# Kernel tuning notes

Measured on AMD Instinct MI355X. Metric: run time of the kernel, lower is better.

The kernel has to match this reference:

```python
import jax, jax.numpy as jnp
import numpy as np

NMS_THR = 0.3


def pairwise_iou(b):
    # b: [N,4] in x1,y1,x2,y2
    area = (b[:, 2] - b[:, 0]) * (b[:, 3] - b[:, 1])  # [N]
    x1 = jnp.maximum(b[:, None, 0], b[None, :, 0])
    y1 = jnp.maximum(b[:, None, 1], b[None, :, 1])
    x2 = jnp.minimum(b[:, None, 2], b[None, :, 2])
    y2 = jnp.minimum(b[:, None, 3], b[None, :, 3])
    inter = jnp.clip(x2 - x1, 0.0) * jnp.clip(y2 - y1, 0.0)
    return inter / (area[:, None] + area[None, :] - inter + 1e-9)


def nms_keep(boxes, scores, valid, thr):
    # greedy NMS, fixed-shape: returns bool keep mask in original order
    N = boxes.shape[0]
    order = jnp.argsort(-jnp.where(valid, scores, -jnp.inf))
    b = boxes[order]
    v = valid[order]
    iou = pairwise_iou(b)  # [N,N]

    def step(keep, i):
        suppressed = jnp.any(keep & (iou[i] > thr))
        keep = keep.at[i].set(v[i] & jnp.logical_not(suppressed))
        return keep, None

    keep_sorted, _ = jax.lax.scan(step, jnp.zeros((N,), dtype=bool), jnp.arange(N))
    return jnp.zeros((N,), dtype=bool).at[order].set(keep_sorted)


def setup_inputs() -> dict:
    key = jax.random.key(0)
    k1, k2, k3, k4 = jax.random.split(key, 4)
    N, C, S = 6000, 81, 800
    # well-formed proposals: x1,y1 in [0, 600), w,h in [8, 200)
    xy = jax.random.uniform(k1, (N, 2), dtype=jnp.float32) * 600.0
    wh = 8.0 + jax.random.uniform(k2, (N, 2), dtype=jnp.float32) * 192.0
    proposals = jnp.concatenate([xy, xy + wh], axis=1)  # [N,4]
    reg = jax.random.normal(k3, (N, C * 4), dtype=jnp.float32)
    clss = jax.random.normal(k4, (N, C), dtype=jnp.float32) * 2.0
    stds = jnp.array([0.1, 0.1, 0.2, 0.2], dtype=jnp.float32)
    return {"proposals": proposals, "reg": reg, "clss": clss, "stds": stds, "img_size": S}


def reference(proposals, reg, clss, stds, img_size):
    N, C = clss.shape
    # anchors_bbox2offset: x1y1x2y2 -> center x,y + w,h
    w = proposals[:, 2] - proposals[:, 0]
    h = proposals[:, 3] - proposals[:, 1]
    cx = proposals[:, 0] + 0.5 * w
    cy = proposals[:, 1] + 0.5 * h
    # class selection
    probs = jax.nn.softmax(clss, axis=1)
    cls_idx = jnp.argmax(probs, axis=1)  # [N]
    score = jnp.take_along_axis(probs, cls_idx[:, None], axis=1)[:, 0]
    valid = cls_idx != 0  # non-background
    reg4 = reg.reshape(N, C, 4)
    t = jnp.take_along_axis(reg4, cls_idx[:, None, None], axis=1)[:, 0, :] * stds  # [N,4]
    # decode
    px = cx + w * t[:, 0]
    py = cy + h * t[:, 1]
    pw = w * jnp.exp(t[:, 2])
    ph = h * jnp.exp(t[:, 3])
    # offset2bbox + clip
    hi = jnp.float32(img_size - 1)
    x1 = jnp.clip(px - 0.5 * pw, 0.0, hi)
    y1 = jnp.clip(py - 0.5 * ph, 0.0, hi)
    x2 = jnp.clip(px + 0.5 * pw, 0.0, hi)
    y2 = jnp.clip(py + 0.5 * ph, 0.0, hi)
    boxes = jnp.stack((x1, y1, x2, y2), axis=1)  # [N,4]
    keep = nms_keep(jax.lax.stop_gradient(boxes), jax.lax.stop_gradient(score), valid, NMS_THR)
    m = keep.astype(boxes.dtype)
    return boxes * m[:, None], score * m, cls_idx * keep.astype(cls_idx.dtype)
```

## Files before the change

kernel.cpp:

```cpp
#include <hip/hip_runtime.h>
#include <math.h>

#define NMS_THR 0.3f
#define NACC 8

__device__ __forceinline__ float fmul(float a, float b){ return __fmul_rn(a,b); }
__device__ __forceinline__ float fadd(float a, float b){ return __fadd_rn(a,b); }
__device__ __forceinline__ float fsub(float a, float b){ return __fsub_rn(a,b); }

#define BAR_LDS() asm volatile("s_waitcnt lgkmcnt(0)\n\ts_barrier" ::: "memory")

__device__ __forceinline__ unsigned long long rfl64(unsigned long long x){
    unsigned int lo = (unsigned int)__builtin_amdgcn_readfirstlane((int)(unsigned int)x);
    unsigned int hi = (unsigned int)__builtin_amdgcn_readfirstlane((int)(unsigned int)(x >> 32));
    return ((unsigned long long)hi << 32) | lo;
}
__device__ __forceinline__ unsigned long long waveOr64(unsigned long long v){
    for (int o = 32; o > 0; o >>= 1) v |= __shfl_xor(v, o);
    return v;
}

__global__ __launch_bounds__(256) void k_decode(
    const float* __restrict__ prop, const float* __restrict__ reg,
    const float* __restrict__ clss, const float* __restrict__ stds,
    const int* __restrict__ imgsz,
    float* __restrict__ boxes, float* __restrict__ key,
    float* __restrict__ score, int* __restrict__ cls,
    int N, int C)
{
    int wid  = threadIdx.x >> 6;
    int lane = threadIdx.x & 63;
    int n = blockIdx.x * 4 + wid;
    if (n >= N) return;
    const float* row = clss + (long)n * C;
    float ninf = -__builtin_inff();
    float x0 = (lane < C)      ? row[lane]      : ninf;
    float x1 = (lane + 64 < C) ? row[lane + 64] : ninf;
    float m = fmaxf(x0, x1);
    for (int o = 32; o > 0; o >>= 1) m = fmaxf(m, __shfl_xor(m, o));
    float e0 = (lane < C)      ? expf(x0 - m) : 0.0f;
    float e1 = (lane + 64 < C) ? expf(x1 - m) : 0.0f;
    float s = e0 + e1;
    for (int o = 32; o > 0; o >>= 1) s += __shfl_xor(s, o);
    float bv; int bi;
    if (e0 >= e1) { bv = e0; bi = lane; } else { bv = e1; bi = lane + 64; }
    for (int o = 32; o > 0; o >>= 1) {
        float ov = __shfl_xor(bv, o);
        int   oi = __shfl_xor(bi, o);
        if (ov > bv || (ov == bv && oi < bi)) { bv = ov; bi = oi; }
    }
    if (lane == 0) {
        float sc = 1.0f / s;
        int   c  = bi;
        int   valid = (c != 0);
        float p0 = prop[n*4+0], p1 = prop[n*4+1], p2 = prop[n*4+2], p3 = prop[n*4+3];
        float w  = fsub(p2, p0), h = fsub(p3, p1);
        float cx = fadd(p0, fmul(0.5f, w));
        float cy = fadd(p1, fmul(0.5f, h));
        const float* rr = reg + (long)n * C * 4 + (long)c * 4;
        float t0 = fmul(rr[0], stds[0]);
        float t1 = fmul(rr[1], stds[1]);
        float t2 = fmul(rr[2], stds[2]);
        float t3 = fmul(rr[3], stds[3]);
        float px = fadd(cx, fmul(w, t0));
        float py = fadd(cy, fmul(h, t1));
        float pw = fmul(w, expf(t2));
        float ph = fmul(h, expf(t3));
        float hi = (float)(imgsz[0] - 1);
        float bx1 = fminf(fmaxf(fsub(px, fmul(0.5f, pw)), 0.0f), hi);
        float by1 = fminf(fmaxf(fsub(py, fmul(0.5f, ph)), 0.0f), hi);
        float bx2 = fminf(fmaxf(fadd(px, fmul(0.5f, pw)), 0.0f), hi);
        float by2 = fminf(fmaxf(fadd(py, fmul(0.5f, ph)), 0.0f), hi);
        boxes[n*4+0]=bx1; boxes[n*4+1]=by1; boxes[n*4+2]=bx2; boxes[n*4+3]=by2;
        score[n] = sc;
        cls[n]   = c;
        key[n]   = valid ? sc : ninf;
    }
}

__global__ __launch_bounds__(256) void k_rank(
    const float* __restrict__ key, const float* __restrict__ boxes,
    float* __restrict__ boxesSorted, float* __restrict__ areaSorted,
    float* __restrict__ keySorted, int* __restrict__ rank,
    int* __restrict__ nValidPtr, int N)
{
    extern __shared__ float lkey[];
    __shared__ int part[256];
    int tid = threadIdx.x;
    for (int j = tid; j < N; j += 256) lkey[j] = key[j];
    __syncthreads();

    int i = blockIdx.x * 64 + (tid & 63);
    int s = tid >> 6;
    int Q = (N + 3) >> 2;
    int r_part = 0;
    if (i < N) {
        float ki = lkey[i];
        int j0 = s * Q, j1 = min(N, j0 + Q);
        for (int j = j0; j < j1; ++j) {
            float kj = lkey[j];
            r_part += (kj > ki) || (kj == ki && j < i);
        }
    }
    part[tid] = r_part;
    __syncthreads();

    if (tid < 64 && i < N) {
        int r = part[tid] + part[tid+64] + part[tid+128] + part[tid+192];
        float ki = lkey[i];
        rank[i] = r;
        float b0 = boxes[i*4+0], b1 = boxes[i*4+1], b2 = boxes[i*4+2], b3 = boxes[i*4+3];
        boxesSorted[r*4+0]=b0; boxesSorted[r*4+1]=b1; boxesSorted[r*4+2]=b2; boxesSorted[r*4+3]=b3;
        areaSorted[r] = fmul(fsub(b2,b0), fsub(b3,b1));
        keySorted[r]  = ki;
    }

    if (blockIdx.x == 0) {
        __syncthreads();
        float ninf = -__builtin_inff();
        int inv = 0;
        for (int j = tid; j < N; j += 256) inv += (lkey[j] == ninf);
        part[tid] = inv;
        __syncthreads();
        if (tid == 0) {
            int t = 0;
            for (int q = 0; q < 256; ++q) t += part[q];
            nValidPtr[0] = N - t;
        }
    }
}

__global__ __launch_bounds__(256) void k_mask(
    const float* __restrict__ bs, const float* __restrict__ areas,
    const float* __restrict__ keySorted, unsigned long long* __restrict__ mask,
    unsigned long long* __restrict__ dq,
    unsigned long long* __restrict__ bdiag, unsigned long long* __restrict__ bprev,
    int N, int W, int Wpad)
{
    int wid  = threadIdx.x >> 6;
    int lane = threadIdx.x & 63;
    int i = blockIdx.x * 4 + wid;
    if (i >= N) return;
    if (keySorted[i] == -__builtin_inff()) return;
    float ax1 = bs[i*4+0], ay1 = bs[i*4+1], ax2 = bs[i*4+2], ay2 = bs[i*4+3];
    float aa  = areas[i];
    int w0 = i >> 6;
    if (lane == 0) {
        dq[i*4+0] = 0ULL; dq[i*4+1] = 0ULL; dq[i*4+2] = 0ULL; dq[i*4+3] = 0ULL;
    }
    if (w0 & 1) {
        int j = (w0 - 1) * 64 + lane;
        int bit = 0;
        if (j < N) {
            float bx1 = bs[j*4+0], by1 = bs[j*4+1], bx2 = bs[j*4+2], by2 = bs[j*4+3];
            float ba  = areas[j];
            float ix1 = fmaxf(ax1,bx1), iy1 = fmaxf(ay1,by1);
            float ix2 = fminf(ax2,bx2), iy2 = fminf(ay2,by2);
            float iw = fmaxf(fsub(ix2,ix1), 0.0f);
            float ih = fmaxf(fsub(iy2,iy1), 0.0f);
            float inter = fmul(iw, ih);
            float denom = fadd(fsub(fadd(aa, ba), inter), 1e-9f);
            float iou = inter / denom;
            bit = (iou > NMS_THR) ? 1 : 0;
        }
        unsigned long long bm = __ballot(bit);
        if (lane == 0) bprev[i] = bm;
    }
    for (int w = w0; w < W; ++w) {
        int j = w*64 + lane;
        int bit = 0;
        if (j < N && j != i) {
            float bx1 = bs[j*4+0], by1 = bs[j*4+1], bx2 = bs[j*4+2], by2 = bs[j*4+3];
            float ba  = areas[j];
            float ix1 = fmaxf(ax1,bx1), iy1 = fmaxf(ay1,by1);
            float ix2 = fminf(ax2,bx2), iy2 = fminf(ay2,by2);
            float iw = fmaxf(fsub(ix2,ix1), 0.0f);
            float ih = fmaxf(fsub(iy2,iy1), 0.0f);
            float inter = fmul(iw, ih);
            float denom = fadd(fsub(fadd(aa, ba), inter), 1e-9f);
            float iou = inter / denom;
            bit = (iou > NMS_THR) ? 1 : 0;
        }
        unsigned long long fwd = __ballot(bit && (j > i));
        if (w == w0) {
            unsigned long long bwd = __ballot(bit && (j < i));
            if (lane == 0) {
                mask[(long)i*Wpad + w] = fwd;
                dq[i*4+0] = fwd;
                bdiag[i]  = bwd;
            }
        } else {
            if (lane == 0) {
                mask[(long)i*Wpad + w] = fwd;
                int d = w - w0;
                if (d < 4) dq[i*4+d] = fwd;
            }
        }
    }
}

__global__ __launch_bounds__((NACC+1)*64, 1) void k_scan(
    const unsigned long long* __restrict__ mask,
    const unsigned long long* __restrict__ dq,
    const unsigned long long* __restrict__ bdiag,
    const unsigned long long* __restrict__ bprev,
    const int* __restrict__ nValidPtr,
    int* __restrict__ keepSorted, int N, int W, int Wpad)
{
    __shared__ unsigned long long ldsPartA[NACC+1];
    __shared__ unsigned long long ldsPartB[NACC+1];
    __shared__ unsigned long long ldsKeepLo, ldsKeepHi;
    int tid  = threadIdx.x;
    int wid  = tid >> 6;
    int lane = tid & 63;
    for (int i = tid; i < N; i += (NACC+1)*64) keepSorted[i] = 0;
    if (tid <= NACC) { ldsPartA[tid] = 0ULL; ldsPartB[tid] = 0ULL; }
    if (tid == 0) { ldsKeepLo = 0ULL; ldsKeepHi = 0ULL; }
    __syncthreads();

    int nValid  = __builtin_amdgcn_readfirstlane(nValidPtr[0]);
    int nChunks = (nValid + 127) >> 7;

    unsigned long long vA=0, vBp=0, vBd=0, A2=0, A3=0, B1=0, B2=0;
    unsigned long long sacc_prevA = 0ULL, sacc_prevB = 0ULL;
    if (wid == 0 && nChunks > 0) {
        int rA = lane, rB = 64 + lane;
        if (rA < N) {
            vA = bdiag[rA];
            ulonglong2 a23 = *(const ulonglong2*)(dq + (size_t)rA*4 + 2);
            A2 = a23.x; A3 = a23.y;
        }
        if (rB < N) {
            vBp = bprev[rB];
            vBd = bdiag[rB];
            ulonglong2 b01 = *(const ulonglong2*)(dq + (size_t)rB*4);
            ulonglong2 b23 = *(const ulonglong2*)(dq + (size_t)rB*4 + 2);
            B1 = b01.y; B2 = b23.x;
        }
    }
    unsigned long long accx = 0ULL, accy = 0ULL;
    bool accWave = (wid >= 1);
    int  accIdx  = wid - 1;
    bool laneok  = (2*lane + 1 < Wpad);

    for (int c = 0; c < nChunks; ++c) {
        int base = c << 7;
        if (wid == 0) {
            unsigned long long nvA=0, nvBp=0, nvBd=0, nA2=0, nA3=0, nB1=0, nB2=0;
            if (c + 1 < nChunks) {
                int rA = base + 128 + lane, rB = base + 192 + lane;
                if (rA < N) {
                    nvA = bdiag[rA];
                    ulonglong2 a23 = *(const ulonglong2*)(dq + (size_t)rA*4 + 2);
                    nA2 = a23.x; nA3 = a23.y;
                }
                if (rB < N) {
                    nvBp = bprev[rB];
                    nvBd = bdiag[rB];
                    ulonglong2 b01 = *(const ulonglong2*)(dq + (size_t)rB*4);
                    ulonglong2 b23 = *(const ulonglong2*)(dq + (size_t)rB*4 + 2);
                    nB1 = b01.y; nB2 = b23.x;
                }
            }

            unsigned long long pA = sacc_prevA, pB = sacc_prevB;
#pragma unroll
            for (int k = 1; k <= NACC; ++k) { pA |= ldsPartA[k]; pB |= ldsPartB[k]; }
            unsigned long long incLo = rfl64(pA), incHi = rfl64(pB);
            int nv  = nValid - base;
            unsigned long long validLo = (nv >= 64) ? ~0ULL : ((1ULL << nv) - 1ULL);
            int nv2 = nv - 64;
            unsigned long long validHi = (nv2 >= 64) ? ~0ULL
                                        : (nv2 <= 0 ? 0ULL : ((1ULL << nv2) - 1ULL));
            unsigned long long candLo = validLo & ~incLo;
            unsigned long long candHi = validHi & ~incHi;
            unsigned long long keepLo = 0ULL, keepHi = 0ULL;

            while (candLo) {
                int f = __builtin_ctzll(candLo);
                unsigned long long sup = __ballot(((vA >> f) & 1ULL) != 0ULL);
                unsigned long long b = 1ULL << f;
                keepLo |= b;
                candLo &= ~sup & ~b;
            }
            candHi &= ~__ballot((vBp & keepLo) != 0ULL);
            while (candHi) {
                int f = __builtin_ctzll(candHi);
                unsigned long long sup = __ballot(((vBd >> f) & 1ULL) != 0ULL);
                unsigned long long b = 1ULL << f;
                keepHi |= b;
                candHi &= ~sup & ~b;
            }
            {
                unsigned long long kL = (keepLo >> lane) & 1ULL;
                unsigned long long kH = (keepHi >> lane) & 1ULL;
                unsigned long long selA = (kL ? A2 : 0ULL) | (kH ? B1 : 0ULL);
                unsigned long long selB = (kL ? A3 : 0ULL) | (kH ? B2 : 0ULL);
                sacc_prevA = waveOr64(selA);
                sacc_prevB = waveOr64(selB);
            }
            if (lane == 0) { ldsKeepLo = keepLo; ldsKeepHi = keepHi; }
            if (base + lane < N)      keepSorted[base + lane]      = (int)((keepLo >> lane) & 1ULL);
            if (base + 64 + lane < N) keepSorted[base + 64 + lane] = (int)((keepHi >> lane) & 1ULL);
            vA=nvA; vBp=nvBp; vBd=nvBd; A2=nA2; A3=nA3; B1=nB1; B2=nB2;
        }
        BAR_LDS();
        unsigned long long kLo = ldsKeepLo;
        unsigned long long kHi = ldsKeepHi;
        if (accWave && laneok && lane == c + 1) {
            ldsPartA[wid] = accx;
            ldsPartB[wid] = accy;
        }
        BAR_LDS();
        if (accWave && laneok) {
            unsigned int myb = (accIdx < 4)
                ? (unsigned int)((kLo >> (16*accIdx)) & 0xFFFFULL)
                : (unsigned int)((kHi >> (16*(accIdx-4))) & 0xFFFFULL);
            if (myb) {
                const unsigned long long* mb =
                    mask + (size_t)(base + 16*accIdx) * Wpad + 2*lane;
                unsigned int b = myb;
                int a0 = __builtin_ctz(b); b &= b - 1;
                int a1=-1,a2=-1,a3=-1,a4=-1,a5=-1,a6=-1,a7=-1;
                if (b) { a1 = __builtin_ctz(b); b &= b - 1; }
                if (b) { a2 = __builtin_ctz(b); b &= b - 1; }
                if (b) { a3 = __builtin_ctz(b); b &= b - 1; }
                if (b) { a4 = __builtin_ctz(b); b &= b - 1; }
                if (b) { a5 = __builtin_ctz(b); b &= b - 1; }
                if (b) { a6 = __builtin_ctz(b); b &= b - 1; }
                if (b) { a7 = __builtin_ctz(b); b &= b - 1; }
                ulonglong2 v0 = {0,0}, v1 = {0,0}, v2 = {0,0}, v3 = {0,0};
                ulonglong2 v4 = {0,0}, v5 = {0,0}, v6 = {0,0}, v7 = {0,0};
                v0 = *(const ulonglong2*)(mb + (size_t)a0 * Wpad);
                if (a1 >= 0) v1 = *(const ulonglong2*)(mb + (size_t)a1 * Wpad);
                if (a2 >= 0) v2 = *(const ulonglong2*)(mb + (size_t)a2 * Wpad);
                if (a3 >= 0) v3 = *(const ulonglong2*)(mb + (size_t)a3 * Wpad);
                if (a4 >= 0) v4 = *(const ulonglong2*)(mb + (size_t)a4 * Wpad);
                if (a5 >= 0) v5 = *(const ulonglong2*)(mb + (size_t)a5 * Wpad);
                if (a6 >= 0) v6 = *(const ulonglong2*)(mb + (size_t)a6 * Wpad);
                if (a7 >= 0) v7 = *(const ulonglong2*)(mb + (size_t)a7 * Wpad);
                accx |= ((v0.x|v1.x)|(v2.x|v3.x)) | ((v4.x|v5.x)|(v6.x|v7.x));
                accy |= ((v0.y|v1.y)|(v2.y|v3.y)) | ((v4.y|v5.y)|(v6.y|v7.y));
                while (b) {
                    int a = __builtin_ctz(b); b &= b - 1;
                    ulonglong2 v = *(const ulonglong2*)(mb + (size_t)a * Wpad);
                    accx |= v.x; accy |= v.y;
                }
            }
        }
    }
}

__global__ __launch_bounds__(256) void k_out(
    const float* __restrict__ boxes, const float* __restrict__ score,
    const int* __restrict__ cls, const int* __restrict__ rank,
    const int* __restrict__ keepSorted,
    float* __restrict__ out, int N)
{
    int n = blockIdx.x * blockDim.x + threadIdx.x;
    if (n >= N) return;
    int k = keepSorted[rank[n]];
    float m = (float)k;
    out[n*4+0] = boxes[n*4+0]*m;
    out[n*4+1] = boxes[n*4+1]*m;
    out[n*4+2] = boxes[n*4+2]*m;
    out[n*4+3] = boxes[n*4+3]*m;
    out[(long)N*4 + n] = score[n]*m;
    out[(long)N*5 + n] = (float)(cls[n] * k);
}

extern "C" void kernel_launch(void* const* d_in, const int* in_sizes, int n_in,
                              void* d_out, int out_size, void* d_ws, size_t ws_size,
                              hipStream_t stream) {
    const float* prop = (const float*)d_in[0];
    const float* reg  = (const float*)d_in[1];
    const float* clss = (const float*)d_in[2];
    const float* stds = (const float*)d_in[3];
    const int*   img  = (const int*)d_in[4];

    int N = in_sizes[0] / 4;
    int C = in_sizes[2] / N;
    int W = (N + 63) / 64;
    int Wpad = (W + 1) & ~1;

    char* ws = (char*)d_ws;
    size_t off = 0;
    float* boxes       = (float*)(ws + off); off += (size_t)N*4*sizeof(float);
    float* key         = (float*)(ws + off); off += (size_t)N*sizeof(float);
    float* score       = (float*)(ws + off); off += (size_t)N*sizeof(float);
    int*   cls         = (int*)  (ws + off); off += (size_t)N*sizeof(int);
    int*   rank        = (int*)  (ws + off); off += (size_t)N*sizeof(int);
    float* boxesSorted = (float*)(ws + off); off += (size_t)N*4*sizeof(float);
    float* areaSorted  = (float*)(ws + off); off += (size_t)N*sizeof(float);
    float* keySorted   = (float*)(ws + off); off += (size_t)N*sizeof(float);
    int*   keepSorted  = (int*)  (ws + off); off += (size_t)N*sizeof(int);
    int*   nValid      = (int*)  (ws + off); off += sizeof(int);
    off = (off + 31) & ~(size_t)31;
    unsigned long long* dq    = (unsigned long long*)(ws + off);
    off += (size_t)N * 4 * sizeof(unsigned long long);
    unsigned long long* bdiag = (unsigned long long*)(ws + off);
    off += (size_t)N * sizeof(unsigned long long);
    unsigned long long* bprev = (unsigned long long*)(ws + off);
    off += (size_t)N * sizeof(unsigned long long);
    unsigned long long* mask  = (unsigned long long*)(ws + off);
    off += (size_t)N * Wpad * sizeof(unsigned long long);
    (void)ws_size; (void)out_size; (void)n_in;

    int rowBlocks  = (N + 3) / 4;
    int thrBlocks  = (N + 255) / 256;
    int rankBlocks = (N + 63) / 64;

    k_decode<<<rowBlocks, 256, 0, stream>>>(prop, reg, clss, stds, img,
                                            boxes, key, score, cls, N, C);
    k_rank<<<rankBlocks, 256, (size_t)N*sizeof(float), stream>>>(key, boxes,
                                            boxesSorted, areaSorted, keySorted, rank, nValid, N);
    k_mask<<<rowBlocks, 256, 0, stream>>>(boxesSorted, areaSorted, keySorted,
                                          mask, dq, bdiag, bprev, N, W, Wpad);
    k_scan<<<1, (NACC+1)*64, 0, stream>>>(mask, dq, bdiag, bprev, nValid,
                                          keepSorted, N, W, Wpad);
    k_out<<<thrBlocks, 256, 0, stream>>>(boxes, score, cls, rank, keepSorted,
                                         (float*)d_out, N);
}
```

Measured before the change: 181.0 us.

## Switch NMS scan lookahead from forward to backward suppression bitmasks

The mask kernel now writes, for each row, backward-looking suppression masks against the same and the three previous 64-column words, instead of forward masks plus separate diagonal and previous arrays. The serial scan wave then computes suppression from the previous chunk with two ballots over the row's own backward masks and the previous keep bits. This replaces the two 6-step shuffle OR reductions on the critical path of the single-block scan. The cost is three extra backward IoU words per row in the mask kernel and a different packed layout for the lookahead data.

Measured after the change: 170.7 us, median of 2. -5.7%, faster.

```diff
diff --git a/kernel.cpp b/kernel.cpp
--- a/kernel.cpp
+++ b/kernel.cpp
@@ -14,10 +14,6 @@
     unsigned int lo = (unsigned int)__builtin_amdgcn_readfirstlane((int)(unsigned int)x);
     unsigned int hi = (unsigned int)__builtin_amdgcn_readfirstlane((int)(unsigned int)(x >> 32));
     return ((unsigned long long)hi << 32) | lo;
-}
-__device__ __forceinline__ unsigned long long waveOr64(unsigned long long v){
-    for (int o = 32; o > 0; o >>= 1) v |= __shfl_xor(v, o);
-    return v;
 }
 
 __global__ __launch_bounds__(256) void k_decode(
@@ -133,8 +129,7 @@
 __global__ __launch_bounds__(256) void k_mask(
     const float* __restrict__ bs, const float* __restrict__ areas,
     const float* __restrict__ keySorted, unsigned long long* __restrict__ mask,
-    unsigned long long* __restrict__ dq,
-    unsigned long long* __restrict__ bdiag, unsigned long long* __restrict__ bprev,
+    unsigned long long* __restrict__ bq,
     int N, int W, int Wpad)
 {
     int wid  = threadIdx.x >> 6;
@@ -145,13 +140,11 @@
     float ax1 = bs[i*4+0], ay1 = bs[i*4+1], ax2 = bs[i*4+2], ay2 = bs[i*4+3];
     float aa  = areas[i];
     int w0 = i >> 6;
-    if (lane == 0) {
-        dq[i*4+0] = 0ULL; dq[i*4+1] = 0ULL; dq[i*4+2] = 0ULL; dq[i*4+3] = 0ULL;
-    }
-    if (w0 & 1) {
-        int j = (w0 - 1) * 64 + lane;
-        int bit = 0;
-        if (j < N) {
+#pragma unroll
+    for (int k = 1; k <= 3; ++k) {
+        unsigned long long bm = 0ULL;
+        if (w0 - k >= 0) {
+            int j = (w0 - k) * 64 + lane;
             float bx1 = bs[j*4+0], by1 = bs[j*4+1], bx2 = bs[j*4+2], by2 = bs[j*4+3];
             float ba  = areas[j];
             float ix1 = fmaxf(ax1,bx1), iy1 = fmaxf(ay1,by1);
@@ -161,10 +154,9 @@
             float inter = fmul(iw, ih);
             float denom = fadd(fsub(fadd(aa, ba), inter), 1e-9f);
             float iou = inter / denom;
-            bit = (iou > NMS_THR) ? 1 : 0;
-        }
-        unsigned long long bm = __ballot(bit);
-        if (lane == 0) bprev[i] = bm;
+            bm = __ballot(iou > NMS_THR);
+        }
+        if (lane == 0) bq[(size_t)i*4 + k] = bm;
     }
     for (int w = w0; w < W; ++w) {
         int j = w*64 + lane;
@@ -186,24 +178,17 @@
             unsigned long long bwd = __ballot(bit && (j < i));
             if (lane == 0) {
                 mask[(long)i*Wpad + w] = fwd;
-                dq[i*4+0] = fwd;
-                bdiag[i]  = bwd;
+                bq[(size_t)i*4 + 0] = bwd;
             }
         } else {
-            if (lane == 0) {
-                mask[(long)i*Wpad + w] = fwd;
-                int d = w - w0;
-                if (d < 4) dq[i*4+d] = fwd;
-            }
+            if (lane == 0) mask[(long)i*Wpad + w] = fwd;
         }
     }
 }
 
 __global__ __launch_bounds__((NACC+1)*64, 1) void k_scan(
     const unsigned long long* __restrict__ mask,
-    const unsigned long long* __restrict__ dq,
-    const unsigned long long* __restrict__ bdiag,
-    const unsigned long long* __restrict__ bprev,
+    const unsigned long long* __restrict__ bq,
     const int* __restrict__ nValidPtr,
     int* __restrict__ keepSorted, int N, int W, int Wpad)
 {
@@ -221,21 +206,19 @@
     int nValid  = __builtin_amdgcn_readfirstlane(nValidPtr[0]);
     int nChunks = (nValid + 127) >> 7;
 
-    unsigned long long vA=0, vBp=0, vBd=0, A2=0, A3=0, B1=0, B2=0;
-    unsigned long long sacc_prevA = 0ULL, sacc_prevB = 0ULL;
+    unsigned long long a0=0,a1=0,a2=0,a3=0, b0=0,b1=0,b2=0,b3=0;
+    unsigned long long keepLoPrev = 0ULL, keepHiPrev = 0ULL;
     if (wid == 0 && nChunks > 0) {
         int rA = lane, rB = 64 + lane;
         if (rA < N) {
-            vA = bdiag[rA];
-            ulonglong2 a23 = *(const ulonglong2*)(dq + (size_t)rA*4 + 2);
-            A2 = a23.x; A3 = a23.y;
+            ulonglong2 q01 = *(const ulonglong2*)(bq + (size_t)rA*4);
+            ulonglong2 q23 = *(const ulonglong2*)(bq + (size_t)rA*4 + 2);
+            a0=q01.x; a1=q01.y; a2=q23.x; a3=q23.y;
         }
         if (rB < N) {
-            vBp = bprev[rB];
-            vBd = bdiag[rB];
-            ulonglong2 b01 = *(const ulonglong2*)(dq + (size_t)rB*4);
-            ulonglong2 b23 = *(const ulonglong2*)(dq + (size_t)rB*4 + 2);
-            B1 = b01.y; B2 = b23.x;
+            ulonglong2 q01 = *(const ulonglong2*)(bq + (size_t)rB*4);
+            ulonglong2 q23 = *(const ulonglong2*)(bq + (size_t)rB*4 + 2);
+            b0=q01.x; b1=q01.y; b2=q23.x; b3=q23.y;
         }
     }
     unsigned long long accx = 0ULL, accy = 0ULL;
@@ -246,27 +229,30 @@
     for (int c = 0; c < nChunks; ++c) {
         int base = c << 7;
         if (wid == 0) {
-            unsigned long long nvA=0, nvBp=0, nvBd=0, nA2=0, nA3=0, nB1=0, nB2=0;
+            unsigned long long na0=0,na1=0,na2=0,na3=0, nb0=0,nb1=0,nb2=0,nb3=0;
             if (c + 1 < nChunks) {
                 int rA = base + 128 + lane, rB = base + 192 + lane;
                 if (rA < N) {
-                    nvA = bdiag[rA];
-                    ulonglong2 a23 = *(const ulonglong2*)(dq + (size_t)rA*4 + 2);
-                    nA2 = a23.x; nA3 = a23.y;
+                    ulonglong2 q01 = *(const ulonglong2*)(bq + (size_t)rA*4);
+                    ulonglong2 q23 = *(const ulonglong2*)(bq + (size_t)rA*4 + 2);
+                    na0=q01.x; na1=q01.y; na2=q23.x; na3=q23.y;
                 }
                 if (rB < N) {
-                    nvBp = bprev[rB];
-                    nvBd = bdiag[rB];
-                    ulonglong2 b01 = *(const ulonglong2*)(dq + (size_t)rB*4);
-                    ulonglong2 b23 = *(const ulonglong2*)(dq + (size_t)rB*4 + 2);
-                    nB1 = b01.y; nB2 = b23.x;
+                    ulonglong2 q01 = *(const ulonglong2*)(bq + (size_t)rB*4);
+                    ulonglong2 q23 = *(const ulonglong2*)(bq + (size_t)rB*4 + 2);
+                    nb0=q01.x; nb1=q01.y; nb2=q23.x; nb3=q23.y;
                 }
             }
 
-            unsigned long long pA = sacc_prevA, pB = sacc_prevB;
+            unsigned long long pA = 0ULL, pB = 0ULL;
 #pragma unroll
             for (int k = 1; k <= NACC; ++k) { pA |= ldsPartA[k]; pB |= ldsPartB[k]; }
-            unsigned long long incLo = rfl64(pA), incHi = rfl64(pB);
+            unsigned long long prevLo =
+                __ballot(((a1 & keepHiPrev) | (a2 & keepLoPrev)) != 0ULL);
+            unsigned long long prevHi =
+                __ballot(((b2 & keepHiPrev) | (b3 & keepLoPrev)) != 0ULL);
+            unsigned long long incLo = rfl64(pA) | prevLo;
+            unsigned long long incHi = rfl64(pB) | prevHi;
             int nv  = nValid - base;
             unsigned long long validLo = (nv >= 64) ? ~0ULL : ((1ULL << nv) - 1ULL);
             int nv2 = nv - 64;
@@ -278,31 +264,24 @@
 
             while (candLo) {
                 int f = __builtin_ctzll(candLo);
-                unsigned long long sup = __ballot(((vA >> f) & 1ULL) != 0ULL);
+                unsigned long long sup = __ballot(((a0 >> f) & 1ULL) != 0ULL);
                 unsigned long long b = 1ULL << f;
                 keepLo |= b;
                 candLo &= ~sup & ~b;
             }
-            candHi &= ~__ballot((vBp & keepLo) != 0ULL);
+            candHi &= ~__ballot((b1 & keepLo) != 0ULL);
             while (candHi) {
                 int f = __builtin_ctzll(candHi);
-                unsigned long long sup = __ballot(((vBd >> f) & 1ULL) != 0ULL);
+                unsigned long long sup = __ballot(((b0 >> f) & 1ULL) != 0ULL);
                 unsigned long long b = 1ULL << f;
                 keepHi |= b;
                 candHi &= ~sup & ~b;
             }
-            {
-                unsigned long long kL = (keepLo >> lane) & 1ULL;
-                unsigned long long kH = (keepHi >> lane) & 1ULL;
-                unsigned long long selA = (kL ? A2 : 0ULL) | (kH ? B1 : 0ULL);
-                unsigned long long selB = (kL ? A3 : 0ULL) | (kH ? B2 : 0ULL);
-                sacc_prevA = waveOr64(selA);
-                sacc_prevB = waveOr64(selB);
-            }
+            keepLoPrev = keepLo; keepHiPrev = keepHi;
             if (lane == 0) { ldsKeepLo = keepLo; ldsKeepHi = keepHi; }
             if (base + lane < N)      keepSorted[base + lane]      = (int)((keepLo >> lane) & 1ULL);
             if (base + 64 + lane < N) keepSorted[base + 64 + lane] = (int)((keepHi >> lane) & 1ULL);
-            vA=nvA; vBp=nvBp; vBd=nvBd; A2=nA2; A3=nA3; B1=nB1; B2=nB2;
+            a0=na0; a1=na1; a2=na2; a3=na3; b0=nb0; b1=nb1; b2=nb2; b3=nb3;
         }
         BAR_LDS();
         unsigned long long kLo = ldsKeepLo;
@@ -320,25 +299,25 @@
                 const unsigned long long* mb =
                     mask + (size_t)(base + 16*accIdx) * Wpad + 2*lane;
                 unsigned int b = myb;
-                int a0 = __builtin_ctz(b); b &= b - 1;
-                int a1=-1,a2=-1,a3=-1,a4=-1,a5=-1,a6=-1,a7=-1;
-                if (b) { a1 = __builtin_ctz(b); b &= b - 1; }
-                if (b) { a2 = __builtin_ctz(b); b &= b - 1; }
-                if (b) { a3 = __builtin_ctz(b); b &= b - 1; }
-                if (b) { a4 = __builtin_ctz(b); b &= b - 1; }
-                if (b) { a5 = __builtin_ctz(b); b &= b - 1; }
-                if (b) { a6 = __builtin_ctz(b); b &= b - 1; }
-                if (b) { a7 = __builtin_ctz(b); b &= b - 1; }
+                int q0 = __builtin_ctz(b); b &= b - 1;
+                int q1=-1,q2=-1,q3=-1,q4=-1,q5=-1,q6=-1,q7=-1;
+                if (b) { q1 = __builtin_ctz(b); b &= b - 1; }
+                if (b) { q2 = __builtin_ctz(b); b &= b - 1; }
+                if (b) { q3 = __builtin_ctz(b); b &= b - 1; }
+                if (b) { q4 = __builtin_ctz(b); b &= b - 1; }
+                if (b) { q5 = __builtin_ctz(b); b &= b - 1; }
+                if (b) { q6 = __builtin_ctz(b); b &= b - 1; }
+                if (b) { q7 = __builtin_ctz(b); b &= b - 1; }
                 ulonglong2 v0 = {0,0}, v1 = {0,0}, v2 = {0,0}, v3 = {0,0};
                 ulonglong2 v4 = {0,0}, v5 = {0,0}, v6 = {0,0}, v7 = {0,0};
-                v0 = *(const ulonglong2*)(mb + (size_t)a0 * Wpad);
-                if (a1 >= 0) v1 = *(const ulonglong2*)(mb + (size_t)a1 * Wpad);
-                if (a2 >= 0) v2 = *(const ulonglong2*)(mb + (size_t)a2 * Wpad);
-                if (a3 >= 0) v3 = *(const ulonglong2*)(mb + (size_t)a3 * Wpad);
-                if (a4 >= 0) v4 = *(const ulonglong2*)(mb + (size_t)a4 * Wpad);
-                if (a5 >= 0) v5 = *(const ulonglong2*)(mb + (size_t)a5 * Wpad);
-                if (a6 >= 0) v6 = *(const ulonglong2*)(mb + (size_t)a6 * Wpad);
-                if (a7 >= 0) v7 = *(const ulonglong2*)(mb + (size_t)a7 * Wpad);
+                v0 = *(const ulonglong2*)(mb + (size_t)q0 * Wpad);
+                if (q1 >= 0) v1 = *(const ulonglong2*)(mb + (size_t)q1 * Wpad);
+                if (q2 >= 0) v2 = *(const ulonglong2*)(mb + (size_t)q2 * Wpad);
+                if (q3 >= 0) v3 = *(const ulonglong2*)(mb + (size_t)q3 * Wpad);
+                if (q4 >= 0) v4 = *(const ulonglong2*)(mb + (size_t)q4 * Wpad);
+                if (q5 >= 0) v5 = *(const ulonglong2*)(mb + (size_t)q5 * Wpad);
+                if (q6 >= 0) v6 = *(const ulonglong2*)(mb + (size_t)q6 * Wpad);
+                if (q7 >= 0) v7 = *(const ulonglong2*)(mb + (size_t)q7 * Wpad);
                 accx |= ((v0.x|v1.x)|(v2.x|v3.x)) | ((v4.x|v5.x)|(v6.x|v7.x));
                 accy |= ((v0.y|v1.y)|(v2.y|v3.y)) | ((v4.y|v5.y)|(v6.y|v7.y));
                 while (b) {
@@ -396,12 +375,8 @@
     int*   keepSorted  = (int*)  (ws + off); off += (size_t)N*sizeof(int);
     int*   nValid      = (int*)  (ws + off); off += sizeof(int);
     off = (off + 31) & ~(size_t)31;
-    unsigned long long* dq    = (unsigned long long*)(ws + off);
+    unsigned long long* bq    = (unsigned long long*)(ws + off);
     off += (size_t)N * 4 * sizeof(unsigned long long);
-    unsigned long long* bdiag = (unsigned long long*)(ws + off);
-    off += (size_t)N * sizeof(unsigned long long);
-    unsigned long long* bprev = (unsigned long long*)(ws + off);
-    off += (size_t)N * sizeof(unsigned long long);
     unsigned long long* mask  = (unsigned long long*)(ws + off);
     off += (size_t)N * Wpad * sizeof(unsigned long long);
     (void)ws_size; (void)out_size; (void)n_in;
@@ -415,9 +390,8 @@
     k_rank<<<rankBlocks, 256, (size_t)N*sizeof(float), stream>>>(key, boxes,
                                             boxesSorted, areaSorted, keySorted, rank, nValid, N);
     k_mask<<<rowBlocks, 256, 0, stream>>>(boxesSorted, areaSorted, keySorted,
-                                          mask, dq, bdiag, bprev, N, W, Wpad);
-    k_scan<<<1, (NACC+1)*64, 0, stream>>>(mask, dq, bdiag, bprev, nValid,
-                                          keepSorted, N, W, Wpad);
+                                          mask, bq, N, W, Wpad);
+    k_scan<<<1, (NACC+1)*64, 0, stream>>>(mask, bq, nValid, keepSorted, N, W, Wpad);
     k_out<<<thrBlocks, 256, 0, stream>>>(boxes, score, cls, rank, keepSorted,
                                          (float*)d_out, N);
 }
```
